# Optimization experiments

Hardware: AMD Instinct MI355X
Metric: run time of the kernel (lower is better)

Reference implementation:

```python
import jax, jax.numpy as jnp
import numpy as np

EPS = 1e-7
MAX_TAN_NORM = 10.0  # safe_expmap0 clamp


def logmap0(x):
    # x: [..., D] Lorentz point, x[..., 0] = time component (>= 1)
    x0 = x[..., :1]
    xs = x[..., 1:]
    d = jnp.arccosh(jnp.clip(x0, 1.0 + EPS, None))          # geodesic distance to origin
    ns = jnp.clip(jnp.linalg.norm(xs, axis=-1, keepdims=True), EPS, None)
    return jnp.concatenate([jnp.zeros_like(x0), d * xs / ns], axis=-1)


def safe_expmap0(u):
    # u: tangent at origin; time component is projected out (proju at origin)
    us = u[..., 1:]
    n = jnp.clip(jnp.linalg.norm(us, axis=-1, keepdims=True), EPS, None)
    nc = jnp.minimum(n, MAX_TAN_NORM)                        # clamp norm for stability
    usc = us * (nc / n)
    return jnp.concatenate([jnp.cosh(nc), jnp.sinh(nc) * usc / nc], axis=-1)


def projx(x):
    # re-project onto the hyperboloid: x0 = sqrt(1 + ||xs||^2)
    xs = x[..., 1:]
    x0 = jnp.sqrt(1.0 + jnp.sum(xs * xs, axis=-1, keepdims=True))
    return jnp.concatenate([x0, xs], axis=-1)


def lorentz_linear(x_hyp, W, b):
    t = logmap0(x_hyp)
    y = t @ W.T + b
    return projx(safe_expmap0(y))


def setup_inputs() -> dict:
    key = jax.random.key(0)
    ks = jax.random.split(key, 8)
    N, D_IN, D_HID, D_OUT = 8192, 1024, 4096, 1024
    s = 0.02
    x_sp = jax.random.normal(ks[0], (N, D_IN), dtype=jnp.float32)
    x_hyp = projx(x_sp)  # valid Lorentz point (time comp overwritten)
    W1 = jax.random.normal(ks[1], (D_HID, D_IN), dtype=jnp.float32) * s
    b1 = jnp.zeros((D_HID,), dtype=jnp.float32)
    W2 = jax.random.normal(ks[2], (D_HID, D_HID), dtype=jnp.float32) * s
    b2 = jnp.zeros((D_HID,), dtype=jnp.float32)
    W3 = jax.random.normal(ks[3], (D_OUT, D_HID), dtype=jnp.float32) * s
    b3 = jnp.zeros((D_OUT,), dtype=jnp.float32)
    return {"x_hyp": x_hyp, "W1": W1, "b1": b1, "W2": W2, "b2": b2, "W3": W3, "b3": b3}


def reference(x_hyp, W1, b1, W2, b2, W3, b3):
    # layers[:-1] with inter-layer logmap0 -> (dropout=identity in eval) -> expmap0 -> projx
    h = lorentz_linear(x_hyp, W1, b1)
    h = projx(safe_expmap0(logmap0(h)))
    h = lorentz_linear(h, W2, b2)
    h = projx(safe_expmap0(logmap0(h)))
    return lorentz_linear(h, W3, b3)
```

## Files before the change

### kernel.cpp

```cpp
#include <hip/hip_runtime.h>
#include <stdint.h>

#define EPSF 1e-7f
#define MAXTAN 10.0f

typedef __bf16 bf16x8 __attribute__((ext_vector_type(8)));
typedef float floatx4 __attribute__((ext_vector_type(4)));
typedef __attribute__((address_space(3))) void lds_void_t;
typedef __attribute__((address_space(1))) void gbl_void_t;

__device__ __forceinline__ unsigned short f2bf(float x) {
  union { float f; uint32_t u; } v; v.f = x;
  uint32_t u = v.u;
  u += 0x7fffu + ((u >> 16) & 1u);
  return (unsigned short)(u >> 16);
}
__device__ __forceinline__ float bf2f(unsigned short h) {
  union { uint32_t u; float f; } v; v.u = ((uint32_t)h) << 16;
  return v.f;
}

__device__ __forceinline__ int sniff_mode(const unsigned short* x) {
  int sane = 0;
  for (int i = 0; i < 128; ++i) {
    unsigned short h = x[i];
    int e = (h >> 7) & 0xFF;
    if ((h & 0x7FFF) == 0 || (e >= 96 && e <= 140)) ++sane;
  }
  return (sane >= 120) ? 1 : 0;
}

__global__ void k_init(const unsigned short* __restrict__ x, int* __restrict__ modeg,
                       const void* __restrict__ b1, const void* __restrict__ b2,
                       const void* __restrict__ b3, float* __restrict__ o1,
                       float* __restrict__ o2, float* __restrict__ o3) {
  __shared__ int mds;
  if (threadIdx.x == 0) {
    int m = sniff_mode(x);
    mds = m;
    if (blockIdx.x == 0) *modeg = m;
  }
  __syncthreads();
  int m = mds;
  int i = blockIdx.x * 256 + threadIdx.x;
  if (i < 4096) o1[i] = m ? bf2f(((const unsigned short*)b1)[i]) : ((const float*)b1)[i];
  if (i < 4096) o2[i] = m ? bf2f(((const unsigned short*)b2)[i]) : ((const float*)b2)[i];
  if (i < 1024) o3[i] = m ? bf2f(((const unsigned short*)b3)[i]) : ((const float*)b3)[i];
}

__global__ void k_prep(const void* __restrict__ xv, unsigned short* __restrict__ xb,
                       float* __restrict__ sc0, float* __restrict__ x0c,
                       const int* __restrict__ mode) {
  const int row = blockIdx.x;
  const int tid = threadIdx.x;
  float4 v;
  if (*mode) {
    ushort4 u = ((const ushort4*)((const unsigned short*)xv + (size_t)row * 1024))[tid];
    v.x = bf2f(u.x); v.y = bf2f(u.y); v.z = bf2f(u.z); v.w = bf2f(u.w);
  } else {
    v = ((const float4*)((const float*)xv + (size_t)row * 1024))[tid];
  }
  ushort4 o;
  o.x = f2bf(v.x); o.y = f2bf(v.y); o.z = f2bf(v.z); o.w = f2bf(v.w);
  ((ushort4*)(xb + (size_t)row * 1024))[tid] = o;

  float s = v.x * v.x + v.y * v.y + v.z * v.z + v.w * v.w;
  if (tid == 0) s -= v.x * v.x;
  for (int off = 32; off; off >>= 1) s += __shfl_down(s, off, 64);
  __shared__ float red[4];
  if ((tid & 63) == 0) red[tid >> 6] = s;
  __syncthreads();
  if (tid == 0) {
    s = red[0] + red[1] + red[2] + red[3];
    float ns = fmaxf(sqrtf(s), EPSF);
    float d = acoshf(fmaxf(v.x, 1.0f + EPSF));
    sc0[row] = d / ns;
    x0c[row] = bf2f(o.x);
  }
}

template<int K8>
__global__ void k_cvtw(const void* __restrict__ in, unsigned short* __restrict__ out,
                       const int* __restrict__ mode, int n8, float* __restrict__ c0) {
  int i = blockIdx.x * 256 + threadIdx.x;
  if (i >= n8) return;
  if (*mode) {
    uint4 g = ((const uint4*)in)[i];
    ((uint4*)out)[i] = g;
    if (i % K8 == 0) c0[i / K8] = bf2f((unsigned short)(g.x & 0xFFFFu));
  } else {
    float4 a = ((const float4*)in)[2 * i];
    float4 b = ((const float4*)in)[2 * i + 1];
    ushort4 oa, ob;
    oa.x = f2bf(a.x); oa.y = f2bf(a.y); oa.z = f2bf(a.z); oa.w = f2bf(a.w);
    ob.x = f2bf(b.x); ob.y = f2bf(b.y); ob.z = f2bf(b.z); ob.w = f2bf(b.w);
    ((ushort4*)out)[2 * i] = oa;
    ((ushort4*)out)[2 * i + 1] = ob;
    if (i % K8 == 0) c0[i / K8] = bf2f(oa.x);
  }
}

template<int NBLK>
__global__ void k_sc(const float* __restrict__ part, const unsigned short* __restrict__ y,
                     int stride, float* __restrict__ sc, float* __restrict__ c0,
                     float* __restrict__ ssout, int nrows) {
  int i = blockIdx.x * 256 + threadIdx.x;
  if (i >= nrows) return;
  float s = 0.f;
#pragma unroll
  for (int j = 0; j < NBLK; ++j) s += part[(size_t)i * NBLK + j];
  float n = fmaxf(sqrtf(fmaxf(s, 0.f)), EPSF);
  sc[i] = fminf(n, MAXTAN) / n;
  c0[i] = bf2f(y[(size_t)i * stride]);
  if (ssout) ssout[i] = s;
}

__global__ void k_final(const unsigned short* __restrict__ y, const float* __restrict__ ss,
                        void* __restrict__ outv, const int* __restrict__ mode) {
  const int row = blockIdx.x;
  const int tid = threadIdx.x;
  float n = fmaxf(sqrtf(fmaxf(ss[row], 0.f)), EPSF);
  float nc = fminf(n, MAXTAN);
  float a = sinhf(nc) / n;
  ushort4 u = ((const ushort4*)(y + (size_t)row * 1024))[tid];
  float4 o;
  o.x = bf2f(u.x) * a; o.y = bf2f(u.y) * a;
  o.z = bf2f(u.z) * a; o.w = bf2f(u.w) * a;
  if (tid == 0) o.x = coshf(nc);
  if (*mode) {
    ushort4 o16;
    o16.x = f2bf(o.x); o16.y = f2bf(o.y); o16.z = f2bf(o.z); o16.w = f2bf(o.w);
    ((ushort4*)outv)[(size_t)row * 256 + tid] = o16;
  } else {
    ((float4*)outv)[(size_t)row * 256 + tid] = o;
  }
}

template<int N, int K, int NBLK, int GX>
__global__ __launch_bounds__(256, 4) void k_gemm_bt(
    const unsigned short* __restrict__ A,
    const unsigned short* __restrict__ B,
    const float* __restrict__ bias,
    const float* __restrict__ sc,
    const float* __restrict__ c0f,
    const float* __restrict__ wc0,
    unsigned short* __restrict__ Cb,
    float* __restrict__ part)
{
  __shared__ __align__(16) unsigned short As[128 * 32];
  __shared__ __align__(16) unsigned short Bs[128 * 32];

  const int tid  = threadIdx.x;
  const int wave = tid >> 6;
  const int lane = tid & 63;
  const int quad = lane >> 4;
  const int m16  = lane & 15;

  const int j = blockIdx.x & 7;
  const int k = blockIdx.x >> 3;
  int bxi, byi;
  if (GX == 32) {
    bxi = 16 * (j & 1) + (k & 15);
    byi = 16 * (j >> 1) + (k >> 4);
  } else {
    bxi = k & 7;
    byi = 8 * j + (k >> 3);
  }
  const int bm = byi * 128;
  const int bn = bxi * 128;

  const int srow = lane >> 2;
  const int scol = (((lane & 3) ^ ((srow >> 1) & 3)) << 3);

  const int wm = (wave >> 1) << 6;
  const int wn = (wave & 1) << 6;

  const int rsw = ((quad ^ ((m16 >> 1) & 3)) << 3);

  const int c0i = wave * 2;
  const unsigned short* ga0 = A + (size_t)(bm + c0i * 16 + srow) * K + scol;
  const unsigned short* ga1 = ga0 + (size_t)16 * K;
  const unsigned short* gb0 = B + (size_t)(bn + c0i * 16 + srow) * K + scol;
  const unsigned short* gb1 = gb0 + (size_t)16 * K;

  floatx4 acc[4][4];
#pragma unroll
  for (int i = 0; i < 4; ++i)
#pragma unroll
    for (int jj = 0; jj < 4; ++jj)
#pragma unroll
      for (int r = 0; r < 4; ++r) acc[i][jj][r] = 0.0f;

  for (int k0 = 0; k0 < K; k0 += 32) {
    __builtin_amdgcn_global_load_lds((gbl_void_t*)(void*)ga0,
                                     (lds_void_t*)(As + c0i * 512), 16, 0, 0);
    __builtin_amdgcn_global_load_lds((gbl_void_t*)(void*)ga1,
                                     (lds_void_t*)(As + c0i * 512 + 512), 16, 0, 0);
    __builtin_amdgcn_global_load_lds((gbl_void_t*)(void*)gb0,
                                     (lds_void_t*)(Bs + c0i * 512), 16, 0, 0);
    __builtin_amdgcn_global_load_lds((gbl_void_t*)(void*)gb1,
                                     (lds_void_t*)(Bs + c0i * 512 + 512), 16, 0, 0);
    ga0 += 32; ga1 += 32; gb0 += 32; gb1 += 32;
    __syncthreads();

    bf16x8 af[4], bfg[4];
#pragma unroll
    for (int t = 0; t < 4; ++t) {
      af[t]  = *(const bf16x8*)(As + (wm + t * 16 + m16) * 32 + rsw);
      bfg[t] = *(const bf16x8*)(Bs + (wn + t * 16 + m16) * 32 + rsw);
    }
#pragma unroll
    for (int mt = 0; mt < 4; ++mt)
#pragma unroll
      for (int nt = 0; nt < 4; ++nt)
        acc[mt][nt] = __builtin_amdgcn_mfma_f32_16x16x32_bf16(af[mt], bfg[nt], acc[mt][nt], 0, 0, 0);
    __syncthreads();
  }

#pragma unroll
  for (int mt = 0; mt < 4; ++mt) {
#pragma unroll
    for (int r = 0; r < 4; ++r) {
      const int gm = bm + wm + mt * 16 + quad * 4 + r;
      const float scv = sc[gm];
      const float c0v = c0f[gm];
      float sq = 0.f;
#pragma unroll
      for (int nt = 0; nt < 4; ++nt) {
        const int gn = bn + wn + nt * 16 + m16;
        float v = scv * (acc[mt][nt][r] - c0v * wc0[gn]) + bias[gn];
        Cb[(size_t)gm * N + gn] = f2bf(v);
        sq += (gn == 0) ? 0.f : v * v;
      }
      sq += __shfl_xor(sq, 1, 64);
      sq += __shfl_xor(sq, 2, 64);
      sq += __shfl_xor(sq, 4, 64);
      sq += __shfl_xor(sq, 8, 64);
      if (m16 == 0) part[(size_t)gm * NBLK + 2 * bxi + (wave & 1)] = sq;
    }
  }
}

template<int N, int K>
__global__ __launch_bounds__(512, 2) void k_gemm256(
    const unsigned short* __restrict__ A,
    const unsigned short* __restrict__ B,
    const float* __restrict__ bias,
    const float* __restrict__ sc,
    const float* __restrict__ c0f,
    const float* __restrict__ wc0,
    unsigned short* __restrict__ Cb,
    float* __restrict__ part)
{
  static_assert(K % 32 == 0 && K / 32 >= 4, "need >=4 K-tiles");
  constexpr int NT = K / 32;
  __shared__ __align__(16) unsigned short S[4][2][8192];

  const int tid  = threadIdx.x;
  const int wave = tid >> 6;
  const int lane = tid & 63;
  const int quad = lane >> 4;
  const int m16  = lane & 15;
  const int wr   = wave >> 2;
  const int wc   = wave & 3;

  const int j = blockIdx.x & 7;
  const int k = blockIdx.x >> 3;
  const int bxi = 8 * (j & 1) + (k & 7);
  const int byi = 8 * (j >> 1) + (k >> 3);
  const int bm = byi * 256;
  const int bn = bxi * 256;

  const int gsw8 = (((tid & 3) ^ ((tid >> 3) & 3)) << 3);
  const unsigned short* gA = A + (size_t)(bm + (tid >> 2)) * K + gsw8;
  const unsigned short* gB = B + (size_t)(bn + (tid >> 2)) * K + gsw8;
  const int ld0 = wave * 512;
  const int ld1 = 4096 + wave * 512;

  const int rsw8 = ((quad ^ ((m16 >> 1) & 3)) << 3);
  const int aoff = (wr * 128 + m16) * 32 + rsw8;
  const int boff = (wc * 64  + m16) * 32 + rsw8;

  floatx4 acc[8][4];
#pragma unroll
  for (int i = 0; i < 8; ++i)
#pragma unroll
    for (int jj = 0; jj < 4; ++jj)
#pragma unroll
      for (int r = 0; r < 4; ++r) acc[i][jj][r] = 0.0f;

#define GLL(SRC, DST) __builtin_amdgcn_global_load_lds((gbl_void_t*)(void*)(SRC), (lds_void_t*)(DST), 16, 0, 0)

#pragma unroll
  for (int tt = 0; tt < 3; ++tt) {
    const unsigned short* pa = gA + tt * 32;
    const unsigned short* pb = gB + tt * 32;
    GLL(pa,                   &S[tt][0][ld0]);
    GLL(pa + (size_t)128 * K, &S[tt][0][ld1]);
    GLL(pb,                   &S[tt][1][ld0]);
    GLL(pb + (size_t)128 * K, &S[tt][1][ld1]);
  }
  asm volatile("s_waitcnt vmcnt(8)" ::: "memory");
  __builtin_amdgcn_s_barrier();

  for (int t = 0; t < NT; ++t) {
    const int slot = t & 3;
    const int s3   = (t + 3) & 3;
    const unsigned short* Asl = &S[slot][0][0];
    const unsigned short* Bsl = &S[slot][1][0];
    const int kt = ((t + 3 < NT) ? (t + 3) : (NT - 1)) * 32;
    const unsigned short* ga = gA + kt;
    const unsigned short* gb = gB + kt;

    GLL(ga,                   &S[s3][0][ld0]);
    GLL(ga + (size_t)128 * K, &S[s3][0][ld1]);
    GLL(gb,                   &S[s3][1][ld0]);
    GLL(gb + (size_t)128 * K, &S[s3][1][ld1]);

    bf16x8 a[4], b[4], a2[4];
#pragma unroll
    for (int f = 0; f < 4; ++f) a[f]  = *(const bf16x8*)(Asl + aoff + f * 512);
#pragma unroll
    for (int n = 0; n < 4; ++n) b[n]  = *(const bf16x8*)(Bsl + boff + n * 512);
#pragma unroll
    for (int f = 0; f < 4; ++f) a2[f] = *(const bf16x8*)(Asl + aoff + 2048 + f * 512);

    __builtin_amdgcn_s_setprio(1);
#pragma unroll
    for (int f = 0; f < 4; ++f)
#pragma unroll
      for (int n = 0; n < 4; ++n)
        acc[f][n] = __builtin_amdgcn_mfma_f32_16x16x32_bf16(a[f], b[n], acc[f][n], 0, 0, 0);
#pragma unroll
    for (int f = 0; f < 4; ++f)
#pragma unroll
      for (int n = 0; n < 4; ++n)
        acc[f + 4][n] = __builtin_amdgcn_mfma_f32_16x16x32_bf16(a2[f], b[n], acc[f + 4][n], 0, 0, 0);
    __builtin_amdgcn_s_setprio(0);

    asm volatile("s_waitcnt vmcnt(8)" ::: "memory");
    __builtin_amdgcn_s_barrier();
  }
#undef GLL

  asm volatile("s_waitcnt vmcnt(0)" ::: "memory");

  const int wm = wr * 128;
  const int wn = wc * 64;
#pragma unroll
  for (int mt = 0; mt < 8; ++mt) {
#pragma unroll
    for (int r = 0; r < 4; ++r) {
      const int gm = bm + wm + mt * 16 + quad * 4 + r;
      const float scv = sc[gm];
      const float c0v = c0f[gm];
      float sq = 0.f;
#pragma unroll
      for (int nt = 0; nt < 4; ++nt) {
        const int gn = bn + wn + nt * 16 + m16;
        float v = scv * (acc[mt][nt][r] - c0v * wc0[gn]) + bias[gn];
        Cb[(size_t)gm * N + gn] = f2bf(v);
        sq += (gn == 0) ? 0.f : v * v;
      }
      sq += __shfl_xor(sq, 1, 64);
      sq += __shfl_xor(sq, 2, 64);
      sq += __shfl_xor(sq, 4, 64);
      sq += __shfl_xor(sq, 8, 64);
      if (m16 == 0) part[(size_t)gm * 64 + bxi * 4 + wc] = sq;
    }
  }
}

extern "C" void kernel_launch(void* const* d_in, const int* in_sizes, int n_in,
                              void* d_out, int out_size, void* d_ws, size_t ws_size,
                              hipStream_t stream) {
  const void* x  = d_in[0];
  const void* W1 = d_in[1];
  const void* b1 = d_in[2];
  const void* W2 = d_in[3];
  const void* b2 = d_in[4];
  const void* W3 = d_in[5];
  const void* b3 = d_in[6];

  const int NR = 8192, DIN = 1024, DH = 4096, DOUT = 1024;

  char* ws = (char*)d_ws;
  size_t off = 0;
  int* mode = (int*)(ws + off);                        off += 256;
  unsigned short* W1b = (unsigned short*)(ws + off);   off += (size_t)DH * DIN * 2;
  unsigned short* W2b = (unsigned short*)(ws + off);   off += (size_t)DH * DH * 2;
  unsigned short* W3b = (unsigned short*)(ws + off);   off += (size_t)DOUT * DH * 2;
  unsigned short* xb  = (unsigned short*)(ws + off);   off += (size_t)NR * DIN * 2;
  unsigned short* y1  = (unsigned short*)(ws + off);   off += (size_t)NR * DH * 2;
  unsigned short* y2  = (unsigned short*)(ws + off);   off += (size_t)NR * DH * 2;
  unsigned short* y3  = (unsigned short*)(ws + off);   off += (size_t)NR * DOUT * 2;
  float* part1 = (float*)(ws + off);                   off += (size_t)NR * 64 * 4;
  float* part2 = (float*)(ws + off);                   off += (size_t)NR * 64 * 4;
  float* part3 = (float*)(ws + off);                   off += (size_t)NR * 16 * 4;
  float* sc0  = (float*)(ws + off);                    off += (size_t)NR * 4;
  float* x0c  = (float*)(ws + off);                    off += (size_t)NR * 4;
  float* sc1  = (float*)(ws + off);                    off += (size_t)NR * 4;
  float* c01  = (float*)(ws + off);                    off += (size_t)NR * 4;
  float* sc2  = (float*)(ws + off);                    off += (size_t)NR * 4;
  float* c02  = (float*)(ws + off);                    off += (size_t)NR * 4;
  float* ss3  = (float*)(ws + off);                    off += (size_t)NR * 4;
  float* w1c0 = (float*)(ws + off);                    off += (size_t)DH * 4;
  float* w2c0 = (float*)(ws + off);                    off += (size_t)DH * 4;
  float* w3c0 = (float*)(ws + off);                    off += (size_t)DOUT * 4;
  float* b1f  = (float*)(ws + off);                    off += (size_t)DH * 4;
  float* b2f  = (float*)(ws + off);                    off += (size_t)DH * 4;
  float* b3f  = (float*)(ws + off);                    off += (size_t)DOUT * 4;

  k_init<<<16, 256, 0, stream>>>((const unsigned short*)x, mode, b1, b2, b3, b1f, b2f, b3f);

  k_cvtw<128><<<(DH * DIN / 8 + 255) / 256, 256, 0, stream>>>(W1, W1b, mode, DH * DIN / 8, w1c0);
  k_cvtw<512><<<(DH * DH  / 8 + 255) / 256, 256, 0, stream>>>(W2, W2b, mode, DH * DH / 8, w2c0);
  k_cvtw<512><<<(DOUT * DH / 8 + 255) / 256, 256, 0, stream>>>(W3, W3b, mode, DOUT * DH / 8, w3c0);

  k_prep<<<NR, 256, 0, stream>>>(x, xb, sc0, x0c, mode);

  k_gemm256<4096, 1024><<<512, 512, 0, stream>>>(
      xb, W1b, b1f, sc0, x0c, w1c0, y1, part1);
  k_sc<64><<<(NR + 255) / 256, 256, 0, stream>>>(part1, y1, DH, sc1, c01, nullptr, NR);

  k_gemm256<4096, 4096><<<512, 512, 0, stream>>>(
      y1, W2b, b2f, sc1, c01, w2c0, y2, part2);
  k_sc<64><<<(NR + 255) / 256, 256, 0, stream>>>(part2, y2, DH, sc2, c02, nullptr, NR);

  k_gemm_bt<1024, 4096, 16, 8><<<512, 256, 0, stream>>>(
      y2, W3b, b3f, sc2, c02, w3c0, y3, part3);
  k_sc<16><<<(NR + 255) / 256, 256, 0, stream>>>(part3, y3, DOUT, sc0, x0c, ss3, NR);

  k_final<<<NR, 256, 0, stream>>>(y3, ss3, d_out, mode);
}
```

Measured before the change: 601.9 us.

## Double-buffer LDS fragments in registers to overlap reads with MFMA

```diff
diff --git a/kernel.cpp b/kernel.cpp
--- a/kernel.cpp
+++ b/kernel.cpp
@@ -252,7 +252,7 @@
     unsigned short* __restrict__ Cb,
     float* __restrict__ part)
 {
-  static_assert(K % 32 == 0 && K / 32 >= 4, "need >=4 K-tiles");
+  static_assert(K % 64 == 0 && K / 32 >= 4, "need even NT >= 4");
   constexpr int NT = K / 32;
   __shared__ __align__(16) unsigned short S[4][2][8192];
 
@@ -300,47 +300,58 @@
     GLL(pb,                   &S[tt][1][ld0]);
     GLL(pb + (size_t)128 * K, &S[tt][1][ld1]);
   }
-  asm volatile("s_waitcnt vmcnt(8)" ::: "memory");
+  asm volatile("s_waitcnt vmcnt(4)" ::: "memory");
   __builtin_amdgcn_s_barrier();
 
-  for (int t = 0; t < NT; ++t) {
-    const int slot = t & 3;
-    const int s3   = (t + 3) & 3;
-    const unsigned short* Asl = &S[slot][0][0];
-    const unsigned short* Bsl = &S[slot][1][0];
-    const int kt = ((t + 3 < NT) ? (t + 3) : (NT - 1)) * 32;
-    const unsigned short* ga = gA + kt;
-    const unsigned short* gb = gB + kt;
-
-    GLL(ga,                   &S[s3][0][ld0]);
-    GLL(ga + (size_t)128 * K, &S[s3][0][ld1]);
-    GLL(gb,                   &S[s3][1][ld0]);
-    GLL(gb + (size_t)128 * K, &S[s3][1][ld1]);
-
-    bf16x8 a[4], b[4], a2[4];
-#pragma unroll
-    for (int f = 0; f < 4; ++f) a[f]  = *(const bf16x8*)(Asl + aoff + f * 512);
-#pragma unroll
-    for (int n = 0; n < 4; ++n) b[n]  = *(const bf16x8*)(Bsl + boff + n * 512);
-#pragma unroll
-    for (int f = 0; f < 4; ++f) a2[f] = *(const bf16x8*)(Asl + aoff + 2048 + f * 512);
-
-    __builtin_amdgcn_s_setprio(1);
-#pragma unroll
-    for (int f = 0; f < 4; ++f)
-#pragma unroll
-      for (int n = 0; n < 4; ++n)
-        acc[f][n] = __builtin_amdgcn_mfma_f32_16x16x32_bf16(a[f], b[n], acc[f][n], 0, 0, 0);
-#pragma unroll
-    for (int f = 0; f < 4; ++f)
-#pragma unroll
-      for (int n = 0; n < 4; ++n)
-        acc[f + 4][n] = __builtin_amdgcn_mfma_f32_16x16x32_bf16(a2[f], b[n], acc[f + 4][n], 0, 0, 0);
-    __builtin_amdgcn_s_setprio(0);
-
-    asm volatile("s_waitcnt vmcnt(8)" ::: "memory");
-    __builtin_amdgcn_s_barrier();
-  }
+  bf16x8 aX[4], bX[4], aY[4], bY[4];
+#pragma unroll
+  for (int f = 0; f < 4; ++f) aX[f] = *(const bf16x8*)(&S[0][0][0] + aoff + f * 512);
+#pragma unroll
+  for (int n = 0; n < 4; ++n) bX[n] = *(const bf16x8*)(&S[0][1][0] + boff + n * 512);
+
+#define ITER(T, AC, BC, AN, BN)                                                        \
+  {                                                                                    \
+    const int slot_ = (T) & 3;                                                         \
+    const int s3_   = ((T) + 3) & 3;                                                   \
+    const int kt_   = ((T) + 3 < NT ? (T) + 3 : NT - 1) * 32;                          \
+    GLL(gA + kt_,                   &S[s3_][0][ld0]);                                  \
+    GLL(gA + kt_ + (size_t)128 * K, &S[s3_][0][ld1]);                                  \
+    GLL(gB + kt_,                   &S[s3_][1][ld0]);                                  \
+    GLL(gB + kt_ + (size_t)128 * K, &S[s3_][1][ld1]);                                  \
+    bf16x8 a2_[4];                                                                     \
+    _Pragma("unroll")                                                                  \
+    for (int f = 0; f < 4; ++f)                                                        \
+      a2_[f] = *(const bf16x8*)(&S[slot_][0][0] + aoff + 2048 + f * 512);              \
+    __builtin_amdgcn_s_setprio(1);                                                     \
+    _Pragma("unroll")                                                                  \
+    for (int f = 0; f < 4; ++f)                                                        \
+      _Pragma("unroll")                                                                \
+      for (int n = 0; n < 4; ++n)                                                      \
+        acc[f][n] = __builtin_amdgcn_mfma_f32_16x16x32_bf16(AC[f], BC[n], acc[f][n], 0, 0, 0); \
+    __builtin_amdgcn_s_setprio(0);                                                     \
+    const int sn_ = ((T) + 1 < NT ? (T) + 1 : NT - 1) & 3;                             \
+    _Pragma("unroll")                                                                  \
+    for (int f = 0; f < 4; ++f)                                                        \
+      AN[f] = *(const bf16x8*)(&S[sn_][0][0] + aoff + f * 512);                        \
+    _Pragma("unroll")                                                                  \
+    for (int n = 0; n < 4; ++n)                                                        \
+      BN[n] = *(const bf16x8*)(&S[sn_][1][0] + boff + n * 512);                        \
+    __builtin_amdgcn_s_setprio(1);                                                     \
+    _Pragma("unroll")                                                                  \
+    for (int f = 0; f < 4; ++f)                                                        \
+      _Pragma("unroll")                                                                \
+      for (int n = 0; n < 4; ++n)                                                      \
+        acc[f + 4][n] = __builtin_amdgcn_mfma_f32_16x16x32_bf16(a2_[f], BC[n], acc[f + 4][n], 0, 0, 0); \
+    __builtin_amdgcn_s_setprio(0);                                                     \
+    asm volatile("s_waitcnt vmcnt(4)" ::: "memory");                                   \
+    __builtin_amdgcn_s_barrier();                                                      \
+  }
+
+  for (int t = 0; t < NT; t += 2) {
+    ITER(t,     aX, bX, aY, bY)
+    ITER(t + 1, aY, bY, aX, bX)
+  }
+#undef ITER
 #undef GLL
 
   asm volatile("s_waitcnt vmcnt(0)" ::: "memory");
```

Measured after the change: 608.7 us. About the same (+1.1%).

## Restructure 256x256 GEMM mainloop into 8-phase ping-pong with 64-K tiles

Applied to the files above, without the earlier changes.

```diff
diff --git a/kernel.cpp b/kernel.cpp
--- a/kernel.cpp
+++ b/kernel.cpp
@@ -242,7 +242,7 @@
 }
 
 template<int N, int K>
-__global__ __launch_bounds__(512, 2) void k_gemm256(
+__global__ __launch_bounds__(512, 2) void k_g8p(
     const unsigned short* __restrict__ A,
     const unsigned short* __restrict__ B,
     const float* __restrict__ bias,
@@ -252,9 +252,10 @@
     unsigned short* __restrict__ Cb,
     float* __restrict__ part)
 {
-  static_assert(K % 32 == 0 && K / 32 >= 4, "need >=4 K-tiles");
-  constexpr int NT = K / 32;
-  __shared__ __align__(16) unsigned short S[4][2][8192];
+  static_assert(K % 128 == 0, "need whole iters of 2x64-K tiles");
+  constexpr int NTILES = K / 64;
+  constexpr int NI = NTILES / 2;
+  __shared__ __align__(16) unsigned short S[2][2][2][128][64];
 
   const int tid  = threadIdx.x;
   const int wave = tid >> 6;
@@ -271,15 +272,31 @@
   const int bm = byi * 256;
   const int bn = bxi * 256;
 
-  const int gsw8 = (((tid & 3) ^ ((tid >> 3) & 3)) << 3);
-  const unsigned short* gA = A + (size_t)(bm + (tid >> 2)) * K + gsw8;
-  const unsigned short* gB = B + (size_t)(bn + (tid >> 2)) * K + gsw8;
-  const int ld0 = wave * 512;
-  const int ld1 = 4096 + wave * 512;
-
-  const int rsw8 = ((quad ^ ((m16 >> 1) & 3)) << 3);
-  const int aoff = (wr * 128 + m16) * 32 + rsw8;
-  const int boff = (wc * 64  + m16) * 32 + rsw8;
+  const int srow = tid >> 3;
+  const int sgr  = (tid & 7) ^ (srow & 7);
+  const unsigned short* pA0g = A + (size_t)(bm + srow) * K + sgr * 8;
+  const unsigned short* pA1g = pA0g + (size_t)64 * K;
+  const unsigned short* pA2g = pA0g + (size_t)128 * K;
+  const unsigned short* pA3g = pA0g + (size_t)192 * K;
+  const unsigned short* pB0g = B + (size_t)(bn + srow) * K + sgr * 8;
+  const unsigned short* pB1g = pB0g + (size_t)64 * K;
+  const unsigned short* pB2g = pB0g + (size_t)128 * K;
+  const unsigned short* pB3g = pB0g + (size_t)192 * K;
+  char* dA = (char*)S + (size_t)(tid >> 3) * 128 + (tid & 7) * 16;
+  char* dB = dA + 32768;
+
+  const int pg0 = (((m16 >> 2) & 1) << 2) | (quad ^ (m16 & 3));
+  const int lb0 = m16 * 128 + pg0 * 16;
+  const int lb1 = lb0 ^ 64;
+  const char* Sb = (const char*)S;
+  const char* pAk0d0 = Sb + wr * 16384 + lb0;
+  const char* pAk1d0 = Sb + wr * 16384 + lb1;
+  const char* pAk0d1 = pAk0d0 + 65536;
+  const char* pAk1d1 = pAk1d0 + 65536;
+  const char* pBk0d0 = Sb + 32768 + (wc >> 1) * 16384 + (wc & 1) * 8192 + lb0;
+  const char* pBk1d0 = Sb + 32768 + (wc >> 1) * 16384 + (wc & 1) * 8192 + lb1;
+  const char* pBk0d1 = pBk0d0 + 65536;
+  const char* pBk1d1 = pBk1d0 + 65536;
 
   floatx4 acc[8][4];
 #pragma unroll
@@ -290,60 +307,71 @@
       for (int r = 0; r < 4; ++r) acc[i][jj][r] = 0.0f;
 
 #define GLL(SRC, DST) __builtin_amdgcn_global_load_lds((gbl_void_t*)(void*)(SRC), (lds_void_t*)(DST), 16, 0, 0)
-
-#pragma unroll
-  for (int tt = 0; tt < 3; ++tt) {
-    const unsigned short* pa = gA + tt * 32;
-    const unsigned short* pb = gB + tt * 32;
-    GLL(pa,                   &S[tt][0][ld0]);
-    GLL(pa + (size_t)128 * K, &S[tt][0][ld1]);
-    GLL(pb,                   &S[tt][1][ld0]);
-    GLL(pb + (size_t)128 * K, &S[tt][1][ld1]);
-  }
-  asm volatile("s_waitcnt vmcnt(8)" ::: "memory");
-  __builtin_amdgcn_s_barrier();
-
-  for (int t = 0; t < NT; ++t) {
-    const int slot = t & 3;
-    const int s3   = (t + 3) & 3;
-    const unsigned short* Asl = &S[slot][0][0];
-    const unsigned short* Bsl = &S[slot][1][0];
-    const int kt = ((t + 3 < NT) ? (t + 3) : (NT - 1)) * 32;
-    const unsigned short* ga = gA + kt;
-    const unsigned short* gb = gB + kt;
-
-    GLL(ga,                   &S[s3][0][ld0]);
-    GLL(ga + (size_t)128 * K, &S[s3][0][ld1]);
-    GLL(gb,                   &S[s3][1][ld0]);
-    GLL(gb + (size_t)128 * K, &S[s3][1][ld1]);
-
-    bf16x8 a[4], b[4], a2[4];
-#pragma unroll
-    for (int f = 0; f < 4; ++f) a[f]  = *(const bf16x8*)(Asl + aoff + f * 512);
-#pragma unroll
-    for (int n = 0; n < 4; ++n) b[n]  = *(const bf16x8*)(Bsl + boff + n * 512);
-#pragma unroll
-    for (int f = 0; f < 4; ++f) a2[f] = *(const bf16x8*)(Asl + aoff + 2048 + f * 512);
-
-    __builtin_amdgcn_s_setprio(1);
-#pragma unroll
-    for (int f = 0; f < 4; ++f)
-#pragma unroll
-      for (int n = 0; n < 4; ++n)
-        acc[f][n] = __builtin_amdgcn_mfma_f32_16x16x32_bf16(a[f], b[n], acc[f][n], 0, 0, 0);
-#pragma unroll
-    for (int f = 0; f < 4; ++f)
-#pragma unroll
-      for (int n = 0; n < 4; ++n)
-        acc[f + 4][n] = __builtin_amdgcn_mfma_f32_16x16x32_bf16(a2[f], b[n], acc[f + 4][n], 0, 0, 0);
-    __builtin_amdgcn_s_setprio(0);
-
-    asm volatile("s_waitcnt vmcnt(8)" ::: "memory");
-    __builtin_amdgcn_s_barrier();
-  }
+#define STGH0(D, COL) { GLL(pA0g + (COL), dA + (D) * 65536);         GLL(pA1g + (COL), dA + (D) * 65536 + 8192); \
+                        GLL(pB0g + (COL), dB + (D) * 65536);         GLL(pB1g + (COL), dB + (D) * 65536 + 8192); }
+#define STGH1(D, COL) { GLL(pA2g + (COL), dA + (D) * 65536 + 16384); GLL(pA3g + (COL), dA + (D) * 65536 + 24576); \
+                        GLL(pB2g + (COL), dB + (D) * 65536 + 16384); GLL(pB3g + (COL), dB + (D) * 65536 + 24576); }
+#define RDA(D, MH, DST) { _Pragma("unroll") for (int f = 0; f < 4; ++f) { \
+    DST[f][0] = *(const bf16x8*)(((D) ? pAk0d1 : pAk0d0) + (MH) * 8192 + f * 2048); \
+    DST[f][1] = *(const bf16x8*)(((D) ? pAk1d1 : pAk1d0) + (MH) * 8192 + f * 2048); } }
+#define RDB(D, NH, DST) { _Pragma("unroll") for (int nt = 0; nt < 2; ++nt) { \
+    DST[nt][0] = *(const bf16x8*)(((D) ? pBk0d1 : pBk0d0) + (NH) * 4096 + nt * 2048); \
+    DST[nt][1] = *(const bf16x8*)(((D) ? pBk1d1 : pBk1d0) + (NH) * 4096 + nt * 2048); } }
+#define MFMAQ(MH, NH, AARR, BARR) { \
+    __builtin_amdgcn_s_setprio(1); \
+    _Pragma("unroll") for (int f = 0; f < 4; ++f) \
+      _Pragma("unroll") for (int nt = 0; nt < 2; ++nt) \
+        _Pragma("unroll") for (int ks = 0; ks < 2; ++ks) \
+          acc[(MH) * 4 + f][(NH) * 2 + nt] = __builtin_amdgcn_mfma_f32_16x16x32_bf16( \
+              AARR[f][ks], BARR[nt][ks], acc[(MH) * 4 + f][(NH) * 2 + nt], 0, 0, 0); \
+    __builtin_amdgcn_s_setprio(0); }
+#define BAR __builtin_amdgcn_s_barrier()
+#define VM4 asm volatile("s_waitcnt vmcnt(4)" ::: "memory")
+
+  STGH0(0, 0) STGH1(0, 0) STGH0(1, 64)
+  VM4;
+  BAR;
+
+  bf16x8 aq[4][2], b0[2][2], b1[2][2];
+
+  for (int i = 0; i < NI; ++i) {
+    const int colE = i * 128;
+    const int colO = colE + 64;
+    const int colE2 = (i < NI - 1) ? colE + 128 : colE;
+    const int colO2 = (i < NI - 1) ? colO + 128 : colO;
+
+    RDA(0, 0, aq) RDB(0, 0, b0)
+    STGH1(1, colO)
+    BAR; MFMAQ(0, 0, aq, b0) BAR;
+    RDB(0, 1, b1)
+    BAR; MFMAQ(0, 1, aq, b1) BAR;
+    RDA(0, 1, aq)
+    BAR; MFMAQ(1, 0, aq, b0) BAR;
+    STGH0(0, colE2)
+    BAR; MFMAQ(1, 1, aq, b1)
+    VM4; BAR;
+    RDA(1, 0, aq) RDB(1, 0, b0)
+    STGH1(0, colE2)
+    BAR; MFMAQ(0, 0, aq, b0) BAR;
+    RDB(1, 1, b1)
+    BAR; MFMAQ(0, 1, aq, b1) BAR;
+    RDA(1, 1, aq)
+    BAR; MFMAQ(1, 0, aq, b0) BAR;
+    STGH0(1, colO2)
+    BAR; MFMAQ(1, 1, aq, b1)
+    VM4; BAR;
+  }
+
+  asm volatile("s_waitcnt vmcnt(0)" ::: "memory");
+
+#undef VM4
+#undef BAR
+#undef MFMAQ
+#undef RDB
+#undef RDA
+#undef STGH1
+#undef STGH0
 #undef GLL
-
-  asm volatile("s_waitcnt vmcnt(0)" ::: "memory");
 
   const int wm = wr * 128;
   const int wn = wc * 64;
@@ -419,11 +447,11 @@
 
   k_prep<<<NR, 256, 0, stream>>>(x, xb, sc0, x0c, mode);
 
-  k_gemm256<4096, 1024><<<512, 512, 0, stream>>>(
+  k_g8p<4096, 1024><<<512, 512, 0, stream>>>(
       xb, W1b, b1f, sc0, x0c, w1c0, y1, part1);
   k_sc<64><<<(NR + 255) / 256, 256, 0, stream>>>(part1, y1, DH, sc1, c01, nullptr, NR);
 
-  k_gemm256<4096, 4096><<<512, 512, 0, stream>>>(
+  k_g8p<4096, 4096><<<512, 512, 0, stream>>>(
       y1, W2b, b2f, sc1, c01, w2c0, y2, part2);
   k_sc<64><<<(NR + 255) / 256, 256, 0, stream>>>(part2, y2, DH, sc2, c02, nullptr, NR);
 
```

Result: no change. 598.2 us (-0.6%).
